# Performance work log

Hardware: AMD Instinct MI355X
Metric: run time of the kernel (lower is better)

Reference implementation:

```python
import jax, jax.numpy as jnp
import numpy as np

N_NODES = 50000
N_EDGES = 800000
N_GRAPHS = 1000
IN_F = 11
H = 128
BN_EPS = 1e-5


def _bn(h, g, b):
    # BatchNorm1d training-mode math (biased variance), no running stats
    m = h.mean(axis=0)
    v = h.var(axis=0)
    return (h - m) * jax.lax.rsqrt(v + BN_EPS) * g + b


def _mlp(h, w1, b1, g1, be1, w2, b2, g2, be2):
    h = jax.nn.relu(_bn(h @ w1 + b1, g1, be1))
    h = jax.nn.relu(_bn(h @ w2 + b2, g2, be2))
    return h


def _gin_agg(h, edge_index):
    # GINConv with eps=0: (1+eps)*x + sum_{j->i} x_j
    msgs = h[edge_index[0]]  # [E, F] gather
    agg = jax.ops.segment_sum(msgs, edge_index[1], num_segments=N_NODES)
    return h + agg


def setup_inputs() -> dict:
    key = jax.random.key(0)
    ks = jax.random.split(key, 24)
    d = {}
    d["x"] = jax.random.normal(ks[0], (N_NODES, IN_F), dtype=jnp.float32)
    d["edge_index"] = jax.random.randint(ks[1], (2, N_EDGES), 0, N_NODES, dtype=jnp.int64)
    d["batch"] = jnp.sort(jax.random.randint(ks[2], (N_NODES,), 0, N_GRAPHS, dtype=jnp.int64))

    dims = [
        ("l1", IN_F, H), ("l2", H, H),            # conv1 MLP
        ("l3", H, 2 * H), ("l4", 2 * H, 2 * H),    # conv2 MLP
        ("l5", 2 * H, 2 * H), ("l6", 2 * H, 2 * H),# conv3 MLP
    ]
    ki = 3
    for name, fi, fo in dims:
        d[name + "w"] = jax.random.normal(ks[ki], (fi, fo), dtype=jnp.float32) * (1.0 / np.sqrt(fi)); ki += 1
        d[name + "b"] = jax.random.normal(ks[ki], (fo,), dtype=jnp.float32) * 0.02; ki += 1
        d[name + "g"] = 1.0 + jax.random.normal(ks[ki], (fo,), dtype=jnp.float32) * 0.02; ki += 1
        d[name + "be"] = jax.random.normal(ks[ki], (fo,), dtype=jnp.float32) * 0.02; ki += 1
        ks = jax.random.split(ks[-1], 24); ki = 0
    d["fw1"] = jax.random.normal(ks[0], (2 * H, H), dtype=jnp.float32) * (1.0 / np.sqrt(2 * H))
    d["fb1"] = jax.random.normal(ks[1], (H,), dtype=jnp.float32) * 0.02
    d["fg"] = 1.0 + jax.random.normal(ks[2], (H,), dtype=jnp.float32) * 0.02
    d["fbe"] = jax.random.normal(ks[3], (H,), dtype=jnp.float32) * 0.02
    d["fw2"] = jax.random.normal(ks[4], (H, 1), dtype=jnp.float32) * (1.0 / np.sqrt(H))
    d["fb2"] = jax.random.normal(ks[5], (1,), dtype=jnp.float32) * 0.02
    return d


def reference(x, edge_index, batch,
              l1w, l1b, l1g, l1be, l2w, l2b, l2g, l2be,
              l3w, l3b, l3g, l3be, l4w, l4b, l4g, l4be,
              l5w, l5b, l5g, l5be, l6w, l6b, l6g, l6be,
              fw1, fb1, fg, fbe, fw2, fb2):
    # conv1 + relu (dropout = identity in eval)
    h = _mlp(_gin_agg(x, edge_index), l1w, l1b, l1g, l1be, l2w, l2b, l2g, l2be)
    h = jax.nn.relu(h)
    # conv2 + relu
    h = _mlp(_gin_agg(h, edge_index), l3w, l3b, l3g, l3be, l4w, l4b, l4g, l4be)
    h = jax.nn.relu(h)
    # conv3 + relu
    h = _mlp(_gin_agg(h, edge_index), l5w, l5b, l5g, l5be, l6w, l6b, l6g, l6be)
    h = jax.nn.relu(h)
    # global_add_pool over graphs
    hg = jax.ops.segment_sum(h, batch, num_segments=N_GRAPHS)  # [G, 256]
    hg = jax.nn.relu(_bn(hg @ fw1 + fb1, fg, fbe))
    out = hg @ fw2 + fb2  # [G, 1]
    return out.reshape(-1)
```

## Files before the change

kernel.cpp:

```cpp
#include <hip/hip_runtime.h>

#define NNODES 50000
#define NEDGES 800000
#define NGRAPHS 1000
#define BN_EPS 1e-5f
#define MPAD 50048

typedef unsigned short us_t;
typedef us_t us8 __attribute__((ext_vector_type(8)));
typedef us_t us4 __attribute__((ext_vector_type(4)));
typedef __bf16 bf16x8 __attribute__((ext_vector_type(8)));
typedef float f32x4 __attribute__((ext_vector_type(4)));

__device__ __forceinline__ float b2f(us_t u) {
    union { unsigned int i; float f; } v;
    v.i = ((unsigned int)u) << 16;
    return v.f;
}
__device__ __forceinline__ us_t f2b(float x) {
    unsigned int u = __float_as_uint(x);
    unsigned int r = u + 0x7FFFu + ((u >> 16) & 1u);
    return (us_t)(r >> 16);
}
__device__ __forceinline__ float h2f(us_t u) {
    _Float16 h;
    __builtin_memcpy(&h, &u, 2);
    return (float)h;
}
__device__ __forceinline__ us_t f2h(float x) {
    _Float16 h = (_Float16)x;
    us_t u;
    __builtin_memcpy(&u, &h, 2);
    return u;
}
__device__ __forceinline__ bf16x8 as_bf(us8 v) {
    union { us8 u; bf16x8 b; } c;
    c.u = v;
    return c.b;
}

__device__ __forceinline__ void glds16(const us_t* g, us_t* l) {
    __builtin_amdgcn_global_load_lds(
        (const __attribute__((address_space(1))) void*)g,
        (__attribute__((address_space(3))) void*)l, 16, 0, 0);
}


__global__ void zero_f32(float* __restrict__ p, int n) {
    int i = blockIdx.x * blockDim.x + threadIdx.x;
    if (i < n) p[i] = 0.f;
}


__global__ void csr_hist(const int* __restrict__ dst, int* __restrict__ deg, int E) {
    int e = blockIdx.x * blockDim.x + threadIdx.x;
    if (e < E) atomicAdd(&deg[dst[e]], 1);
}

__global__ void csr_scan1(const int* __restrict__ deg, int* __restrict__ tmpscan,
                          int* __restrict__ chunkTot, int n) {
    __shared__ int sm[1024];
    int i = blockIdx.x * 1024 + threadIdx.x;
    int v = (i < n) ? deg[i] : 0;
    sm[threadIdx.x] = v;
    __syncthreads();
    for (int off = 1; off < 1024; off <<= 1) {
        int add = (threadIdx.x >= off) ? sm[threadIdx.x - off] : 0;
        __syncthreads();
        sm[threadIdx.x] += add;
        __syncthreads();
    }
    if (i < n) tmpscan[i] = sm[threadIdx.x];
    if (threadIdx.x == 1023) chunkTot[blockIdx.x] = sm[1023];
}

__global__ void csr_scan3(const int* __restrict__ deg, const int* __restrict__ tmpscan,
                          const int* __restrict__ chunkTot, int* __restrict__ rowptr,
                          int* __restrict__ cursor, int n, int nchunks) {
    __shared__ int sct[64];
    if (threadIdx.x < nchunks) sct[threadIdx.x] = chunkTot[threadIdx.x];
    __syncthreads();
    int i = blockIdx.x * blockDim.x + threadIdx.x;
    if (i < n) {
        int chunk = i >> 10;
        int pre = 0;
        for (int c = 0; c < chunk; c++) pre += sct[c];
        int inc = tmpscan[i] + pre;
        rowptr[i + 1] = inc;
        cursor[i] = inc - deg[i];
        if (i == 0) rowptr[0] = 0;
    }
}

__global__ void csr_fill(const int* __restrict__ src, const int* __restrict__ dst,
                         int* __restrict__ cursor, int* __restrict__ eidx, int E) {
    int e = blockIdx.x * blockDim.x + threadIdx.x;
    if (e < E) {
        int pos = atomicAdd(&cursor[dst[e]], 1);
        eidx[pos] = src[e];
    }
}


__global__ void wt_convert_all(const float* __restrict__ w2, const float* __restrict__ w3,
                               const float* __restrict__ w4, const float* __restrict__ w5,
                               const float* __restrict__ w6,
                               us_t* __restrict__ o2, us_t* __restrict__ o3,
                               us_t* __restrict__ o4, us_t* __restrict__ o5,
                               us_t* __restrict__ o6) {
    int i = blockIdx.x * blockDim.x + threadIdx.x;
    if (i < 16384) {
        int k = i >> 7, n = i & 127;
        o2[n * 128 + k] = f2b(w2[i]);
    } else if (i < 49152) {
        int j = i - 16384; int k = j >> 8, n = j & 255;
        o3[n * 128 + k] = f2b(w3[j]);
    } else if (i < 114688) {
        int j = i - 49152; int k = j >> 8, n = j & 255;
        o4[n * 256 + k] = f2b(w4[j]);
    } else if (i < 180224) {
        int j = i - 114688; int k = j >> 8, n = j & 255;
        o5[n * 256 + k] = f2b(w5[j]);
    } else if (i < 245760) {
        int j = i - 180224; int k = j >> 8, n = j & 255;
        o6[n * 256 + k] = f2b(w6[j]);
    }
}


__global__ void gin_gather_bn128(const us_t* __restrict__ z, const float* __restrict__ sums,
                                 const float* __restrict__ sumsq, const float* __restrict__ gw,
                                 const float* __restrict__ bw, float invM,
                                 const int* __restrict__ rowptr, const int* __restrict__ eidx,
                                 us_t* __restrict__ out) {
    int ln = threadIdx.x >> 4;
    int fp = threadIdx.x & 15;
    int n = blockIdx.x * 16 + ln;
    if (n >= NNODES) return;
    int f0 = fp * 8;
    float s[8], t[8];
    #pragma unroll
    for (int q = 0; q < 8; q++) {
        float m = sums[f0 + q] * invM;
        float va = sumsq[f0 + q] * invM - m * m;
        s[q] = gw[f0 + q] * rsqrtf(va + BN_EPS);
        t[q] = bw[f0 + q] - m * s[q];
    }
    const us_t* zf = z + f0;
    float a[8];
    us8 v = *(const us8*)&zf[(size_t)n * 128];
    #pragma unroll
    for (int q = 0; q < 8; q++) a[q] = fmaxf(0.f, b2f(v[q]) * s[q] + t[q]);
    int p0 = rowptr[n], p1 = rowptr[n + 1];
    int p = p0;
    for (; p + 4 <= p1; p += 4) {
        int e0 = eidx[p], e1 = eidx[p + 1], e2 = eidx[p + 2], e3 = eidx[p + 3];
        us8 u0 = *(const us8*)&zf[(size_t)e0 * 128];
        us8 u1 = *(const us8*)&zf[(size_t)e1 * 128];
        us8 u2 = *(const us8*)&zf[(size_t)e2 * 128];
        us8 u3 = *(const us8*)&zf[(size_t)e3 * 128];
        #pragma unroll
        for (int q = 0; q < 8; q++)
            a[q] += fmaxf(0.f, b2f(u0[q]) * s[q] + t[q]) +
                    fmaxf(0.f, b2f(u1[q]) * s[q] + t[q]) +
                    fmaxf(0.f, b2f(u2[q]) * s[q] + t[q]) +
                    fmaxf(0.f, b2f(u3[q]) * s[q] + t[q]);
    }
    for (; p < p1; p++) {
        us8 u = *(const us8*)&zf[(size_t)eidx[p] * 128];
        #pragma unroll
        for (int q = 0; q < 8; q++) a[q] += fmaxf(0.f, b2f(u[q]) * s[q] + t[q]);
    }
    us8 o;
    #pragma unroll
    for (int q = 0; q < 8; q++) o[q] = f2b(a[q]);
    *(us8*)&out[(size_t)n * 128 + f0] = o;
}


__global__ void gin_gather_bn256(const us_t* __restrict__ z, const float* __restrict__ sums,
                                 const float* __restrict__ sumsq, const float* __restrict__ gw,
                                 const float* __restrict__ bw, float invM,
                                 const int* __restrict__ rowptr, const int* __restrict__ eidx,
                                 us_t* __restrict__ out) {
    int ln = threadIdx.x >> 5;
    int fp = threadIdx.x & 31;
    int n = blockIdx.x * 8 + ln;
    if (n >= NNODES) return;
    int f0 = fp * 8;
    float s[8], t[8];
    #pragma unroll
    for (int q = 0; q < 8; q++) {
        float m = sums[f0 + q] * invM;
        float va = sumsq[f0 + q] * invM - m * m;
        s[q] = gw[f0 + q] * rsqrtf(va + BN_EPS);
        t[q] = bw[f0 + q] - m * s[q];
    }
    const us_t* zf = z + f0;
    float a[8];
    us8 v = *(const us8*)&zf[(size_t)n * 256];
    #pragma unroll
    for (int q = 0; q < 8; q++) a[q] = fmaxf(0.f, b2f(v[q]) * s[q] + t[q]);
    int p0 = rowptr[n], p1 = rowptr[n + 1];
    int p = p0;
    for (; p + 4 <= p1; p += 4) {
        int e0 = eidx[p], e1 = eidx[p + 1], e2 = eidx[p + 2], e3 = eidx[p + 3];
        us8 u0 = *(const us8*)&zf[(size_t)e0 * 256];
        us8 u1 = *(const us8*)&zf[(size_t)e1 * 256];
        us8 u2 = *(const us8*)&zf[(size_t)e2 * 256];
        us8 u3 = *(const us8*)&zf[(size_t)e3 * 256];
        #pragma unroll
        for (int q = 0; q < 8; q++)
            a[q] += fmaxf(0.f, b2f(u0[q]) * s[q] + t[q]) +
                    fmaxf(0.f, b2f(u1[q]) * s[q] + t[q]) +
                    fmaxf(0.f, b2f(u2[q]) * s[q] + t[q]) +
                    fmaxf(0.f, b2f(u3[q]) * s[q] + t[q]);
    }
    for (; p < p1; p++) {
        us8 u = *(const us8*)&zf[(size_t)eidx[p] * 256];
        #pragma unroll
        for (int q = 0; q < 8; q++) a[q] += fmaxf(0.f, b2f(u[q]) * s[q] + t[q]);
    }
    us8 o;
    #pragma unroll
    for (int q = 0; q < 8; q++) o[q] = f2b(a[q]);
    *(us8*)&out[(size_t)n * 256 + f0] = o;
}

__global__ void gin_gather11(const float* __restrict__ x, const int* __restrict__ rowptr,
                             const int* __restrict__ eidx, float* __restrict__ out) {
    int local = threadIdx.x >> 4;
    int lane = threadIdx.x & 15;
    int n = blockIdx.x * 16 + local;
    if (n >= NNODES) return;
    int p0 = rowptr[n], p1 = rowptr[n + 1];
    float acc = (lane < 11) ? x[n * 11 + lane] : 0.f;
    for (int p = p0; p < p1; p++) {
        int src = eidx[p];
        if (lane < 11) acc += x[src * 11 + lane];
    }
    if (lane < 11) out[n * 11 + lane] = acc;
}


__global__ __launch_bounds__(256) void gemm11(const float* __restrict__ A,
                                              const float* __restrict__ W,
                                              const float* __restrict__ b,
                                              us_t* __restrict__ C,
                                              float* __restrict__ sums,
                                              float* __restrict__ sumsq) {
    __shared__ float sW[11 * 128];
    __shared__ float sArows[64 * 11];
    int tid = threadIdx.x;
    for (int i = tid; i < 11 * 128; i += 256) sW[i] = W[i];
    int r0 = blockIdx.x * 64;
    for (int i = tid; i < 64 * 11; i += 256) {
        int r = i / 11, c = i - r * 11;
        sArows[i] = (r0 + r < NNODES) ? A[(r0 + r) * 11 + c] : 0.f;
    }
    __syncthreads();
    int col = tid & 127;
    int half = tid >> 7;
    float bias = b[col];
    float cs = 0.f, cq = 0.f;
    for (int rr = half * 32; rr < half * 32 + 32; rr++) {
        int row = r0 + rr;
        if (row < NNODES) {
            float acc = bias;
            #pragma unroll
            for (int k = 0; k < 11; k++) acc += sArows[rr * 11 + k] * sW[k * 128 + col];
            C[(size_t)row * 128 + col] = f2h(acc);
            cs += acc;
            cq += acc * acc;
        }
    }
    __syncthreads();
    sArows[tid] = cs;
    sArows[256 + tid] = cq;
    __syncthreads();
    if (tid < 128) {
        atomicAdd(&sums[tid], sArows[tid] + sArows[tid + 128]);
        atomicAdd(&sumsq[tid], sArows[256 + tid] + sArows[256 + tid + 128]);
    }
}


template <int K_, int AMODE, int OMODE, int COLS>
__global__ __launch_bounds__(256, 4) void gemm_v8(
    const void* __restrict__ Ap, const us_t* __restrict__ Wt,
    const float* __restrict__ bias,
    const float* __restrict__ sums_in, const float* __restrict__ sumsq_in,
    const float* __restrict__ gma, const float* __restrict__ bet, float invM,
    us_t* __restrict__ Cp, float* __restrict__ sums, float* __restrict__ sumsq,
    int M, int N, int nrows) {
    __shared__ us_t sAB[2 * 128 * 32];
    __shared__ float sST[(AMODE >= 1) ? 2 * K_ : 2];
    us_t* sA = sAB;
    us_t* sB = sAB + 128 * 32;

    int rowblk, colblk;
    if (COLS == 1) {
        rowblk = blockIdx.x;
        colblk = 0;
    } else {
        int g = blockIdx.x;
        rowblk = (g >> 4) * 8 + (g & 7);
        colblk = (g >> 3) & 1;
        if (rowblk >= nrows) return;
    }
    const int bm = rowblk * 128;
    const int bn = colblk * 128;

    const int tid = threadIdx.x;
    const int lane = tid & 63;
    const int wave = tid >> 6;
    const int wm = wave >> 1, wn = wave & 1;
    const int lrow = lane & 15, lquad = lane >> 4;

    if (AMODE >= 1) {
        if (tid < K_) {
            float m = sums_in[tid] * invM;
            float va = sumsq_in[tid] * invM - m * m;
            float sc = gma[tid] * rsqrtf(va + BN_EPS);
            sST[tid] = sc;
            sST[K_ + tid] = bet[tid] - m * sc;
        }
        __syncthreads();
    }

    f32x4 acc[4][4] = {};

    const int r0c = tid >> 2, q0c = tid & 3;
    const int r1c = (tid + 256) >> 2, q1c = tid & 3;

    #pragma unroll
    for (int kt = 0; kt < K_ / 32; kt++) {
        const int k0 = kt * 32;

        us8 pk[2];
        if (AMODE >= 1) {
            #pragma unroll
            for (int i = 0; i < 2; i++) {
                int row = (i == 0) ? r0c : r1c;
                int kq = (i == 0) ? q0c : q1c;
                int kk = k0 + kq * 8;
                float v[8];
                if (AMODE == 1) {
                    const float* ar = &((const float*)Ap)[(size_t)(bm + row) * K_ + kk];
                    float4 v0 = *(const float4*)ar;
                    float4 v1 = *(const float4*)(ar + 4);
                    v[0] = v0.x; v[1] = v0.y; v[2] = v0.z; v[3] = v0.w;
                    v[4] = v1.x; v[5] = v1.y; v[6] = v1.z; v[7] = v1.w;
                } else {
                    us8 u = *(const us8*)&((const us_t*)Ap)[(size_t)(bm + row) * K_ + kk];
                    #pragma unroll
                    for (int q = 0; q < 8; q++) v[q] = h2f(u[q]);
                }
                float4 s0 = *(const float4*)&sST[kk];
                float4 s1 = *(const float4*)&sST[kk + 4];
                float4 t0 = *(const float4*)&sST[K_ + kk];
                float4 t1 = *(const float4*)&sST[K_ + kk + 4];
                us8 o;
                o[0] = f2b(fmaxf(0.f, v[0] * s0.x + t0.x));
                o[1] = f2b(fmaxf(0.f, v[1] * s0.y + t0.y));
                o[2] = f2b(fmaxf(0.f, v[2] * s0.z + t0.z));
                o[3] = f2b(fmaxf(0.f, v[3] * s0.w + t0.w));
                o[4] = f2b(fmaxf(0.f, v[4] * s1.x + t1.x));
                o[5] = f2b(fmaxf(0.f, v[5] * s1.y + t1.y));
                o[6] = f2b(fmaxf(0.f, v[6] * s1.z + t1.z));
                o[7] = f2b(fmaxf(0.f, v[7] * s1.w + t1.w));
                pk[i] = o;
            }
        }

        __syncthreads();

        {
            glds16(&Wt[(size_t)(bn + r0c) * K_ + k0 + q0c * 8], &sB[(wave * 64) * 8]);
            glds16(&Wt[(size_t)(bn + r1c) * K_ + k0 + q1c * 8], &sB[(256 + wave * 64) * 8]);
        }
        if (AMODE == 0) {
            const us_t* A = (const us_t*)Ap;
            glds16(&A[(size_t)(bm + r0c) * K_ + k0 + q0c * 8], &sA[(wave * 64) * 8]);
            glds16(&A[(size_t)(bm + r1c) * K_ + k0 + q1c * 8], &sA[(256 + wave * 64) * 8]);
        } else {
            *(us8*)&sA[(size_t)tid * 8] = pk[0];
            *(us8*)&sA[(size_t)(tid + 256) * 8] = pk[1];
        }

        __syncthreads();

        bf16x8 af[4], bfr[4];
        #pragma unroll
        for (int i = 0; i < 4; i++)
            af[i] = as_bf(*(const us8*)&sA[(wm * 64 + i * 16 + lrow) * 32 + lquad * 8]);
        #pragma unroll
        for (int j = 0; j < 4; j++)
            bfr[j] = as_bf(*(const us8*)&sB[(wn * 64 + j * 16 + lrow) * 32 + lquad * 8]);
        #pragma unroll
        for (int i = 0; i < 4; i++)
            #pragma unroll
            for (int j = 0; j < 4; j++)
                acc[i][j] = __builtin_amdgcn_mfma_f32_16x16x32_bf16(af[i], bfr[j],
                                                                    acc[i][j], 0, 0, 0);
    }

    __syncthreads();
    float* pf = (float*)sAB;
    #pragma unroll
    for (int j = 0; j < 4; j++) {
        int coll = wn * 64 + j * 16 + lrow;
        float bcol = bias[bn + coll];
        float cs = 0.f, cq = 0.f;
        #pragma unroll
        for (int i = 0; i < 4; i++) {
            int rb = bm + wm * 64 + i * 16 + lquad * 4;
            #pragma unroll
            for (int r = 0; r < 4; r++) {
                if (rb + r < M) {
                    float zv = acc[i][j][r] + bcol;
                    cs += zv;
                    cq += zv * zv;
                }
            }
        }
        cs += __shfl_xor(cs, 16); cs += __shfl_xor(cs, 32);
        cq += __shfl_xor(cq, 16); cq += __shfl_xor(cq, 32);
        if (lquad == 0) {
            pf[wm * 128 + coll] = cs;
            pf[256 + wm * 128 + coll] = cq;
        }
    }
    __syncthreads();
    if (tid < 128) {
        atomicAdd(&sums[bn + tid], pf[tid] + pf[128 + tid]);
        atomicAdd(&sumsq[bn + tid], pf[256 + tid] + pf[384 + tid]);
    }

    #pragma unroll
    for (int p = 0; p < 2; p++) {
        __syncthreads();
        if (wm == p) {
            #pragma unroll
            for (int j = 0; j < 4; j++) {
                int coll = wn * 64 + j * 16 + lrow;
                float bcol = bias[bn + coll];
                #pragma unroll
                for (int i = 0; i < 4; i++) {
                    int rl = i * 16 + lquad * 4;
                    #pragma unroll
                    for (int r = 0; r < 4; r++) {
                        float zv = acc[i][j][r] + bcol;
                        sAB[(rl + r) * 128 + coll] = (OMODE == 0) ? f2b(zv) : f2h(zv);
                    }
                }
            }
        }
        __syncthreads();
        #pragma unroll
        for (int k = 0; k < 4; k++) {
            int c = tid + 256 * k;
            int row = c >> 4, cw = c & 15;
            int grow = bm + p * 64 + row;
            if (grow < M)
                *(us8*)&Cp[(size_t)grow * N + bn + cw * 8] =
                    *(const us8*)&sAB[row * 128 + cw * 8];
        }
    }
}


__global__ void pool_bn_h(const us_t* __restrict__ z, const float* __restrict__ sums,
                          const float* __restrict__ sumsq, const float* __restrict__ gw,
                          const float* __restrict__ bw, float invM,
                          const int* __restrict__ batch, float* __restrict__ hg) {
    int f = threadIdx.x;
    float m = sums[f] * invM;
    float va = sumsq[f] * invM - m * m;
    float sv = gw[f] * rsqrtf(va + BN_EPS);
    float tv = bw[f] - m * sv;
    int n0 = blockIdx.x * 32;
    int n1 = min(n0 + 32, NNODES);
    float acc = 0.f;
    int gc = batch[n0];
    for (int n = n0; n < n1; n++) {
        int g = batch[n];
        if (g != gc) {
            atomicAdd(&hg[gc * 256 + f], acc);
            acc = 0.f;
            gc = g;
        }
        acc += fmaxf(0.f, h2f(z[(size_t)n * 256 + f]) * sv + tv);
    }
    atomicAdd(&hg[gc * 256 + f], acc);
}


#define GBM 128
#define GBN 128
#define GBK 16
#define LDA 132

__global__ __launch_bounds__(256) void gemm_f32_head(
    const float* __restrict__ A, const float* __restrict__ W, const float* __restrict__ bias,
    float* __restrict__ C, float* __restrict__ sums, float* __restrict__ sumsq,
    int M, int K, int N) {
    __shared__ float smem[2 * GBK * LDA];
    float* As = smem;
    float* Ws = smem + GBK * LDA;

    const int bm = blockIdx.y * GBM;
    const int bn = blockIdx.x * GBN;
    const int tid = threadIdx.x;
    const int tm = tid >> 4;
    const int tn = tid & 15;

    float acc[2][2][4][4] = {};

    for (int k0 = 0; k0 < K; k0 += GBK) {
        #pragma unroll
        for (int i = 0; i < 2; i++) {
            int id = tid + 256 * i;
            int row = id >> 2;
            int kq = id & 3;
            int gr = bm + row;
            int kk = k0 + kq * 4;
            float4 a4 = make_float4(0.f, 0.f, 0.f, 0.f);
            if (gr < M && kk < K) a4 = *(const float4*)&A[(size_t)gr * K + kk];
            As[(kq * 4 + 0) * LDA + row] = a4.x;
            As[(kq * 4 + 1) * LDA + row] = a4.y;
            As[(kq * 4 + 2) * LDA + row] = a4.z;
            As[(kq * 4 + 3) * LDA + row] = a4.w;
        }
        #pragma unroll
        for (int i = 0; i < 2; i++) {
            int id = tid + 256 * i;
            int kl = id >> 5;
            int c = id & 31;
            int kk = k0 + kl;
            float4 w4 = make_float4(0.f, 0.f, 0.f, 0.f);
            if (kk < K && bn + c * 4 < N) w4 = *(const float4*)&W[(size_t)kk * N + bn + c * 4];
            *(float4*)&Ws[kl * LDA + c * 4] = w4;
        }
        __syncthreads();
        #pragma unroll
        for (int k = 0; k < GBK; k++) {
            float4 a0 = *(float4*)&As[k * LDA + tm * 4];
            float4 a1 = *(float4*)&As[k * LDA + 64 + tm * 4];
            float4 w0 = *(float4*)&Ws[k * LDA + tn * 4];
            float4 w1 = *(float4*)&Ws[k * LDA + 64 + tn * 4];
            float ar[2][4] = {{a0.x, a0.y, a0.z, a0.w}, {a1.x, a1.y, a1.z, a1.w}};
            float wr[2][4] = {{w0.x, w0.y, w0.z, w0.w}, {w1.x, w1.y, w1.z, w1.w}};
            #pragma unroll
            for (int ri = 0; ri < 2; ri++)
                #pragma unroll
                for (int ci = 0; ci < 2; ci++)
                    #pragma unroll
                    for (int ii = 0; ii < 4; ii++)
                        #pragma unroll
                        for (int jj = 0; jj < 4; jj++)
                            acc[ri][ci][ii][jj] += ar[ri][ii] * wr[ci][jj];
        }
        __syncthreads();
    }

    float colsum[2][4] = {};
    float colsq[2][4] = {};
    #pragma unroll
    for (int ci = 0; ci < 2; ci++) {
        int colbase = bn + ci * 64 + tn * 4;
        if (colbase >= N) continue;
        float4 b4 = *(const float4*)&bias[colbase];
        float br[4] = {b4.x, b4.y, b4.z, b4.w};
        #pragma unroll
        for (int ri = 0; ri < 2; ri++) {
            #pragma unroll
            for (int ii = 0; ii < 4; ii++) {
                int row = bm + ri * 64 + tm * 4 + ii;
                if (row < M) {
                    float z0 = acc[ri][ci][ii][0] + br[0];
                    float z1 = acc[ri][ci][ii][1] + br[1];
                    float z2 = acc[ri][ci][ii][2] + br[2];
                    float z3 = acc[ri][ci][ii][3] + br[3];
                    *(float4*)&C[(size_t)row * N + colbase] = make_float4(z0, z1, z2, z3);
                    colsum[ci][0] += z0; colsq[ci][0] += z0 * z0;
                    colsum[ci][1] += z1; colsq[ci][1] += z1 * z1;
                    colsum[ci][2] += z2; colsq[ci][2] += z2 * z2;
                    colsum[ci][3] += z3; colsq[ci][3] += z3 * z3;
                }
            }
        }
    }
    __syncthreads();
    float* ps = smem;
    float* pq = smem + 2048;
    #pragma unroll
    for (int ci = 0; ci < 2; ci++)
        #pragma unroll
        for (int jj = 0; jj < 4; jj++) {
            int cl = ci * 64 + tn * 4 + jj;
            ps[tm * 128 + cl] = colsum[ci][jj];
            pq[tm * 128 + cl] = colsq[ci][jj];
        }
    __syncthreads();
    if (tid < 128 && bn + tid < N) {
        float s = 0.f, q = 0.f;
        #pragma unroll
        for (int i = 0; i < 16; i++) {
            s += ps[i * 128 + tid];
            q += pq[i * 128 + tid];
        }
        atomicAdd(&sums[bn + tid], s);
        atomicAdd(&sumsq[bn + tid], q);
    }
}


__global__ void final_gemv_raw(const float* __restrict__ hg2, const float* __restrict__ sums,
                               const float* __restrict__ sumsq, const float* __restrict__ gw,
                               const float* __restrict__ bw, float invM,
                               const float* __restrict__ fw2, const float* __restrict__ fb2,
                               float* __restrict__ out) {
    int g = blockIdx.x;
    int l = threadIdx.x;
    float m0 = sums[l] * invM, va0 = sumsq[l] * invM - m0 * m0;
    float s0 = gw[l] * rsqrtf(va0 + BN_EPS), t0 = bw[l] - m0 * s0;
    float m1 = sums[64 + l] * invM, va1 = sumsq[64 + l] * invM - m1 * m1;
    float s1 = gw[64 + l] * rsqrtf(va1 + BN_EPS), t1 = bw[64 + l] - m1 * s1;
    float a0 = fmaxf(0.f, hg2[g * 128 + l] * s0 + t0) * fw2[l];
    float a1 = fmaxf(0.f, hg2[g * 128 + 64 + l] * s1 + t1) * fw2[64 + l];
    float v = a0 + a1;
    #pragma unroll
    for (int o = 32; o > 0; o >>= 1) v += __shfl_down(v, o);
    if (l == 0) out[g] = v + fb2[0];
}


extern "C" void kernel_launch(void* const* d_in, const int* in_sizes, int n_in,
                              void* d_out, int out_size, void* d_ws, size_t ws_size,
                              hipStream_t stream) {
    const float* x = (const float*)d_in[0];
    const int* ei = (const int*)d_in[1];
    const int* batch = (const int*)d_in[2];
    const int* esrc = ei;
    const int* edst = ei + NEDGES;

    const float* l1w = (const float*)d_in[3],  *l1b = (const float*)d_in[4],
               * l1g = (const float*)d_in[5],  *l1be = (const float*)d_in[6];
    const float* l2w = (const float*)d_in[7],  *l2b = (const float*)d_in[8],
               * l2g = (const float*)d_in[9],  *l2be = (const float*)d_in[10];
    const float* l3w = (const float*)d_in[11], *l3b = (const float*)d_in[12],
               * l3g = (const float*)d_in[13], *l3be = (const float*)d_in[14];
    const float* l4w = (const float*)d_in[15], *l4b = (const float*)d_in[16],
               * l4g = (const float*)d_in[17], *l4be = (const float*)d_in[18];
    const float* l5w = (const float*)d_in[19], *l5b = (const float*)d_in[20],
               * l5g = (const float*)d_in[21], *l5be = (const float*)d_in[22];
    const float* l6w = (const float*)d_in[23], *l6b = (const float*)d_in[24],
               * l6g = (const float*)d_in[25], *l6be = (const float*)d_in[26];
    const float* fw1 = (const float*)d_in[27], *fb1 = (const float*)d_in[28],
               * fg  = (const float*)d_in[29], *fbe = (const float*)d_in[30];
    const float* fw2 = (const float*)d_in[31], *fb2 = (const float*)d_in[32];

    us_t* F0h = (us_t*)d_ws;
    us_t* Ba = F0h + (size_t)MPAD * 256;
    us_t* Bz = Ba + (size_t)MPAD * 256;
    us_t* wt2 = Bz + (size_t)MPAD * 256;
    us_t* wt3 = wt2 + 128 * 128;
    us_t* wt4 = wt3 + 256 * 128;
    us_t* wt5 = wt4 + 256 * 256;
    us_t* wt6 = wt5 + 256 * 256;
    float* agg11 = (float*)(wt6 + 256 * 256);
    float* hg = agg11 + (size_t)NNODES * 11;
    float* hg2 = hg + NGRAPHS * 256;
    float* stats = hg2 + NGRAPHS * 128;
    int* deg = (int*)(stats + 7 * 512);
    int* rowptr = deg + (NNODES + 1);
    int* cursor = rowptr + (NNODES + 1);
    int* chunkTot = cursor + (NNODES + 1);
    int* tmpscan = chunkTot + 64;
    int* eidx = tmpscan + (NNODES + 1);

    {
        int zn = NGRAPHS * 256 + NGRAPHS * 128 + 7 * 512 + (NNODES + 1);
        zero_f32<<<(zn + 255) / 256, 256, 0, stream>>>(hg, zn);
    }

    csr_hist<<<(NEDGES + 255) / 256, 256, 0, stream>>>(edst, deg, NEDGES);
    int nchunks = (NNODES + 1023) / 1024;
    csr_scan1<<<nchunks, 1024, 0, stream>>>(deg, tmpscan, chunkTot, NNODES);
    csr_scan3<<<(NNODES + 255) / 256, 256, 0, stream>>>(deg, tmpscan, chunkTot, rowptr,
                                                        cursor, NNODES, nchunks);
    csr_fill<<<(NEDGES + 255) / 256, 256, 0, stream>>>(esrc, edst, cursor, eidx, NEDGES);

    wt_convert_all<<<(245760 + 255) / 256, 256, 0, stream>>>(l2w, l3w, l4w, l5w, l6w,
                                                             wt2, wt3, wt4, wt5, wt6);

    auto st = [&](int i) { return stats + i * 512; };
    const float invN = 1.0f / (float)NNODES;
    const float invG = 1.0f / (float)NGRAPHS;
    const int NRB = MPAD / 128;
    const int NSWZ = ((NRB + 7) / 8) * 16;

    gin_gather11<<<(NNODES + 15) / 16, 256, 0, stream>>>(x, rowptr, eidx, agg11);
    gemm11<<<(NNODES + 63) / 64, 256, 0, stream>>>(agg11, l1w, l1b, F0h, st(0), st(0) + 256);
    gemm_v8<128, 2, 0, 1><<<NRB, 256, 0, stream>>>(
        F0h, wt2, l2b, st(0), st(0) + 256, l1g, l1be, invN,
        Bz, st(1), st(1) + 256, NNODES, 128, NRB);

    gin_gather_bn128<<<(NNODES + 15) / 16, 256, 0, stream>>>(
        Bz, st(1), st(1) + 256, l2g, l2be, invN, rowptr, eidx, Ba);
    gemm_v8<128, 0, 2, 2><<<NSWZ, 256, 0, stream>>>(
        Ba, wt3, l3b, nullptr, nullptr, nullptr, nullptr, 0.f,
        F0h, st(2), st(2) + 256, NNODES, 256, NRB);
    gemm_v8<256, 2, 0, 2><<<NSWZ, 256, 0, stream>>>(
        F0h, wt4, l4b, st(2), st(2) + 256, l3g, l3be, invN,
        Bz, st(3), st(3) + 256, NNODES, 256, NRB);

    gin_gather_bn256<<<(NNODES + 7) / 8, 256, 0, stream>>>(
        Bz, st(3), st(3) + 256, l4g, l4be, invN, rowptr, eidx, Ba);
    gemm_v8<256, 0, 2, 2><<<NSWZ, 256, 0, stream>>>(
        Ba, wt5, l5b, nullptr, nullptr, nullptr, nullptr, 0.f,
        F0h, st(4), st(4) + 256, NNODES, 256, NRB);
    gemm_v8<256, 2, 2, 2><<<NSWZ, 256, 0, stream>>>(
        F0h, wt6, l6b, st(4), st(4) + 256, l5g, l5be, invN,
        Bz, st(5), st(5) + 256, NNODES, 256, NRB);

    pool_bn_h<<<(NNODES + 31) / 32, 256, 0, stream>>>(
        Bz, st(5), st(5) + 256, l6g, l6be, invN, batch, hg);
    gemm_f32_head<<<dim3(1, 8), 256, 0, stream>>>(hg, fw1, fb1, hg2, st(6), st(6) + 256,
                                                  NGRAPHS, 256, 128);
    final_gemv_raw<<<NGRAPHS, 64, 0, stream>>>(hg2, st(6), st(6) + 256, fg, fbe, invG,
                                               fw2, fb2, (float*)d_out);
}
```

Before: 541.9 us.

## Vectorize pooling loads and raise gemm_v8 occupancy hint

The pooling kernel is reorganized so each thread handles four features with a 4-wide vector load, and each block of 256 threads splits its 32 nodes into four chunks of 8. This shortens the serial per-thread loop and widens memory accesses. It increases atomic traffic because each chunk flushes its partial sums separately. Separately, gemm_v8's launch bounds minimum-blocks hint goes from 4 to 6, which may force fewer registers and risk spills.

After: 737.1 us. +36.0%, slower.

```diff
diff --git a/kernel.cpp b/kernel.cpp
--- a/kernel.cpp
+++ b/kernel.cpp
@@ -286,7 +286,7 @@
 
 
 template <int K_, int AMODE, int OMODE, int COLS>
-__global__ __launch_bounds__(256, 4) void gemm_v8(
+__global__ __launch_bounds__(256, 6) void gemm_v8(
     const void* __restrict__ Ap, const us_t* __restrict__ Wt,
     const float* __restrict__ bias,
     const float* __restrict__ sums_in, const float* __restrict__ sumsq_in,
@@ -474,25 +474,37 @@
                           const float* __restrict__ sumsq, const float* __restrict__ gw,
                           const float* __restrict__ bw, float invM,
                           const int* __restrict__ batch, float* __restrict__ hg) {
-    int f = threadIdx.x;
-    float m = sums[f] * invM;
-    float va = sumsq[f] * invM - m * m;
-    float sv = gw[f] * rsqrtf(va + BN_EPS);
-    float tv = bw[f] - m * sv;
-    int n0 = blockIdx.x * 32;
-    int n1 = min(n0 + 32, NNODES);
-    float acc = 0.f;
+    int ln = threadIdx.x >> 6;
+    int fp = threadIdx.x & 63;
+    int f0 = fp * 4;
+    float s[4], t[4];
+    #pragma unroll
+    for (int q = 0; q < 4; q++) {
+        float m = sums[f0 + q] * invM;
+        float va = sumsq[f0 + q] * invM - m * m;
+        s[q] = gw[f0 + q] * rsqrtf(va + BN_EPS);
+        t[q] = bw[f0 + q] - m * s[q];
+    }
+    int n0 = blockIdx.x * 32 + ln * 8;
+    int n1 = min(n0 + 8, NNODES);
+    if (n0 >= NNODES) return;
+    float a[4] = {};
     int gc = batch[n0];
     for (int n = n0; n < n1; n++) {
         int g = batch[n];
         if (g != gc) {
-            atomicAdd(&hg[gc * 256 + f], acc);
-            acc = 0.f;
+            #pragma unroll
+            for (int q = 0; q < 4; q++) atomicAdd(&hg[gc * 256 + f0 + q], a[q]);
+            #pragma unroll
+            for (int q = 0; q < 4; q++) a[q] = 0.f;
             gc = g;
         }
-        acc += fmaxf(0.f, h2f(z[(size_t)n * 256 + f]) * sv + tv);
-    }
-    atomicAdd(&hg[gc * 256 + f], acc);
+        us4 v = *(const us4*)&z[(size_t)n * 256 + f0];
+        #pragma unroll
+        for (int q = 0; q < 4; q++) a[q] += fmaxf(0.f, h2f(v[q]) * s[q] + t[q]);
+    }
+    #pragma unroll
+    for (int q = 0; q < 4; q++) atomicAdd(&hg[gc * 256 + f0 + q], a[q]);
 }
 
 
```
